# Optimization experiments

Measured on AMD Instinct MI355X. Metric: run time of the kernel, lower is better.

The kernel has to match this reference:

```python
import jax, jax.numpy as jnp
import numpy as np
import math

B, T, S, C, H = 2, 2048, 2048, 1024, 16
D = C // H  # head dim = 64


def setup_inputs() -> dict:
    key = jax.random.key(0)
    ks = jax.random.split(key, 12)
    s = 1.0 / math.sqrt(C)
    inp = {
        "query": jax.random.normal(ks[0], (B, T, C), jnp.float32),
        "key": jax.random.normal(ks[1], (B, S, C), jnp.float32),
        "value": jax.random.normal(ks[2], (B, S, C), jnp.float32),
        "Wq": jax.random.normal(ks[3], (C, C), jnp.float32) * s,
        "bq": jax.random.normal(ks[4], (C,), jnp.float32) * s,
        "Wk": jax.random.normal(ks[5], (C, C), jnp.float32) * s,
        "bk": jax.random.normal(ks[6], (C,), jnp.float32) * s,
        "Wv": jax.random.normal(ks[7], (C, C), jnp.float32) * s,
        "bv": jax.random.normal(ks[8], (C,), jnp.float32) * s,
        "Wo": jax.random.normal(ks[9], (C, C), jnp.float32) * s,
        "bo": jax.random.normal(ks[10], (C,), jnp.float32) * s,
        "query_chunk_size": 1024,
    }
    return inp


def _proj_heads(x, W, b):
    # x: [B, L, C] -> [B, H, L, D]; torch nn.Linear computes x @ W.T + b
    y = x @ W.T + b
    Bv, L, _ = y.shape
    return y.reshape(Bv, L, H, D).transpose(0, 2, 1, 3)


def reference(query, key, value, Wq, bq, Wk, bk, Wv, bv, Wo, bo, query_chunk_size):
    # query_chunk_size only controls the chunked evaluation order in the
    # original; the chunked online-softmax is mathematically identical to a
    # single stable softmax, which is what we compute here.
    q = _proj_heads(query, Wq, bq) * (1.0 / math.sqrt(D))  # [B,H,T,D]
    k = _proj_heads(key, Wk, bk)                            # [B,H,S,D]
    v = _proj_heads(value, Wv, bv)                          # [B,H,S,D]
    scores = jnp.einsum('bhqd,bhkd->bhqk', q, k)            # [B,H,T,S]
    attn = jax.nn.softmax(scores, axis=-1)
    out = jnp.einsum('bhqk,bhkd->bhqd', attn, v)            # [B,H,T,D]
    out = out.transpose(0, 2, 1, 3).reshape(query.shape[0], query.shape[1], C)
    return out @ Wo.T + bo
```

## Files before the change

kernel.cpp:

```cpp
#include <hip/hip_runtime.h>
#include <math.h>


typedef __attribute__((ext_vector_type(4))) float f32x4;
typedef __attribute__((ext_vector_type(8))) __bf16 bf16x8;
typedef __attribute__((ext_vector_type(4))) unsigned int u32x4;
typedef __attribute__((ext_vector_type(4))) unsigned short u16x4;

#define MFMA16(a, b, c) __builtin_amdgcn_mfma_f32_16x16x32_bf16(a, b, c, 0, 0, 0)

static __device__ __forceinline__ unsigned short f2bf(float f) {
    __bf16 h = (__bf16)f;
    return __builtin_bit_cast(unsigned short, h);
}

__global__ __launch_bounds__(256, 2)
void proj_qkv_kernel(const float* __restrict__ Xq, const float* __restrict__ Xk,
                     const float* __restrict__ Xv,
                     const float* __restrict__ Wq, const float* __restrict__ Wk,
                     const float* __restrict__ Wv,
                     const float* __restrict__ bq, const float* __restrict__ bk,
                     const float* __restrict__ bv,
                     unsigned short* __restrict__ qh, unsigned short* __restrict__ kh,
                     unsigned short* __restrict__ vh)
{
    const int z = blockIdx.z;
    const float* X    = (z == 0) ? Xq : (z == 1) ? Xk : Xv;
    const float* W    = (z == 0) ? Wq : (z == 1) ? Wk : Wv;
    const float* bias = (z == 0) ? bq : (z == 1) ? bk : bv;
    unsigned short* O = (z == 0) ? qh : (z == 1) ? kh : vh;
    const float scale = (z == 0) ? 0.125f : 1.0f;

    __shared__ unsigned short As[128 * 32];
    __shared__ unsigned short Bs[128 * 32];

    const int tid  = threadIdx.x;
    const int lane = tid & 63;
    const int w    = tid >> 6;
    const int l16  = lane & 15;
    const int quad = lane >> 4;
    const int wm   = (w >> 1) * 64;
    const int wn   = (w & 1) * 64;
    const int m0   = blockIdx.y * 128;
    const int n0   = blockIdx.x * 128;

    const int srow = tid >> 3;
    const int sc4  = tid & 7;

    f32x4 acc[4][4];
#pragma unroll
    for (int i = 0; i < 4; i++)
#pragma unroll
        for (int j = 0; j < 4; j++) {
            f32x4 zv = {0.0f, 0.0f, 0.0f, 0.0f};
            acc[i][j] = zv;
        }

    for (int k0 = 0; k0 < 1024; k0 += 32) {
#pragma unroll
        for (int rr = 0; rr < 4; rr++) {
            int row = rr * 32 + srow;
            f32x4 xa = *(const f32x4*)(X + (size_t)(m0 + row) * 1024 + k0 + sc4 * 4);
            f32x4 xb = *(const f32x4*)(W + (size_t)(n0 + row) * 1024 + k0 + sc4 * 4);
            u16x4 ha, hb;
#pragma unroll
            for (int e = 0; e < 4; e++) { ha[e] = f2bf(xa[e]); hb[e] = f2bf(xb[e]); }
            *(u16x4*)(As + row * 32 + sc4 * 4) = ha;
            *(u16x4*)(Bs + row * 32 + sc4 * 4) = hb;
        }
        __syncthreads();

        bf16x8 af[4], bfr[4];
#pragma unroll
        for (int mi = 0; mi < 4; mi++)
            af[mi] = *(const bf16x8*)(As + (wm + mi * 16 + l16) * 32 + quad * 8);
#pragma unroll
        for (int ni = 0; ni < 4; ni++)
            bfr[ni] = *(const bf16x8*)(Bs + (wn + ni * 16 + l16) * 32 + quad * 8);
#pragma unroll
        for (int mi = 0; mi < 4; mi++)
#pragma unroll
            for (int ni = 0; ni < 4; ni++)
                acc[mi][ni] = MFMA16(af[mi], bfr[ni], acc[mi][ni]);
        __syncthreads();
    }

#pragma unroll
    for (int ni = 0; ni < 4; ni++) {
        int gn = n0 + wn + ni * 16 + l16;
        float bval = bias[gn];
        int h = gn >> 6, d = gn & 63;
#pragma unroll
        for (int mi = 0; mi < 4; mi++) {
#pragma unroll
            for (int r = 0; r < 4; r++) {
                int gm = m0 + wm + mi * 16 + quad * 4 + r;
                int b = gm >> 11, l = gm & 2047;
                float val = (acc[mi][ni][r] + bval) * scale;
                O[(((size_t)(b * 16 + h) * 2048 + l) * 64) + d] = f2bf(val);
            }
        }
    }
}

__global__ __launch_bounds__(256, 2)
void attn_kernel(const unsigned short* __restrict__ qh,
                 const unsigned short* __restrict__ kh,
                 const unsigned short* __restrict__ vh,
                 unsigned short* __restrict__ ao)
{
    __shared__ unsigned short Vt[64 * 144];
    __shared__ unsigned short Ps[128 * 136];

    const int tid  = threadIdx.x;
    const int lane = tid & 63;
    const int w    = tid >> 6;
    const int l16  = lane & 15;
    const int quad = lane >> 4;
    const int qt   = blockIdx.x;
    const int bh   = blockIdx.y;

    const unsigned short* Qb = qh + (size_t)bh * 2048 * 64;
    const unsigned short* Kb = kh + (size_t)bh * 2048 * 64;
    const unsigned short* Vb = vh + (size_t)bh * 2048 * 64;

    bf16x8 qf[2][2];
#pragma unroll
    for (int mi = 0; mi < 2; mi++)
#pragma unroll
        for (int ks = 0; ks < 2; ks++)
            qf[mi][ks] = *(const bf16x8*)(Qb +
                (size_t)(qt * 128 + w * 32 + mi * 16 + l16) * 64 + ks * 32 + quad * 8);

    f32x4 o[2][4];
    float mrow[2][4], lrow[2][4];
#pragma unroll
    for (int mi = 0; mi < 2; mi++) {
#pragma unroll
        for (int di = 0; di < 4; di++) {
            f32x4 zv = {0.0f, 0.0f, 0.0f, 0.0f};
            o[mi][di] = zv;
        }
#pragma unroll
        for (int r = 0; r < 4; r++) { mrow[mi][r] = -__builtin_inff(); lrow[mi][r] = 0.0f; }
    }

    for (int s0 = 0; s0 < 2048; s0 += 128) {
        __syncthreads();

#pragma unroll
        for (int r = 0; r < 2; r++) {
            int p  = r * 256 + tid;
            int d0 = (p & 7) * 8;
            int sr = (p >> 3) * 2;
            const unsigned short* src = Vb + (size_t)(s0 + sr) * 64 + d0;
            u32x4 a  = *(const u32x4*)(src);
            u32x4 b2 = *(const u32x4*)(src + 64);
            unsigned int aw[4] = {a[0], a[1], a[2], a[3]};
            unsigned int bw[4] = {b2[0], b2[1], b2[2], b2[3]};
#pragma unroll
            for (int j = 0; j < 8; j++) {
                int i = (j + (p & 7)) & 7;
                unsigned int lo = (i & 1) ? (aw[i >> 1] >> 16) : (aw[i >> 1] & 0xffffu);
                unsigned int hi = (i & 1) ? (bw[i >> 1] >> 16) : (bw[i >> 1] & 0xffffu);
                *(unsigned int*)(Vt + (d0 + i) * 144 + sr) = lo | (hi << 16);
            }
        }
        __syncthreads();

        f32x4 sacc[2][8];
#pragma unroll
        for (int mi = 0; mi < 2; mi++)
#pragma unroll
            for (int ni = 0; ni < 8; ni++) {
                f32x4 zv = {0.0f, 0.0f, 0.0f, 0.0f};
                sacc[mi][ni] = zv;
            }
#pragma unroll
        for (int ni = 0; ni < 8; ni++) {
#pragma unroll
            for (int ks = 0; ks < 2; ks++) {
                bf16x8 kf = *(const bf16x8*)(Kb +
                    (size_t)(s0 + ni * 16 + l16) * 64 + ks * 32 + quad * 8);
                sacc[0][ni] = MFMA16(qf[0][ks], kf, sacc[0][ni]);
                sacc[1][ni] = MFMA16(qf[1][ks], kf, sacc[1][ni]);
            }
        }

#pragma unroll
        for (int mi = 0; mi < 2; mi++) {
#pragma unroll
            for (int r = 0; r < 4; r++) {
                float mx = sacc[mi][0][r];
#pragma unroll
                for (int ni = 1; ni < 8; ni++) mx = fmaxf(mx, sacc[mi][ni][r]);
#pragma unroll
                for (int off = 1; off < 16; off <<= 1)
                    mx = fmaxf(mx, __shfl_xor(mx, off, 64));
                float mnew  = fmaxf(mrow[mi][r], mx);
                float alpha = __expf(mrow[mi][r] - mnew);
                mrow[mi][r] = mnew;
                float sum = 0.0f;
                int prow = w * 32 + mi * 16 + quad * 4 + r;
#pragma unroll
                for (int ni = 0; ni < 8; ni++) {
                    float pv = __expf(sacc[mi][ni][r] - mnew);
                    sum += pv;
                    Ps[prow * 136 + ni * 16 + l16] = f2bf(pv);
                }
#pragma unroll
                for (int off = 1; off < 16; off <<= 1)
                    sum += __shfl_xor(sum, off, 64);
                lrow[mi][r] = lrow[mi][r] * alpha + sum;
#pragma unroll
                for (int di = 0; di < 4; di++) o[mi][di][r] *= alpha;
            }
        }

#pragma unroll
        for (int kk = 0; kk < 4; kk++) {
            bf16x8 pf[2];
#pragma unroll
            for (int mi = 0; mi < 2; mi++)
                pf[mi] = *(const bf16x8*)(Ps + (w * 32 + mi * 16 + l16) * 136 + kk * 32 + quad * 8);
#pragma unroll
            for (int di = 0; di < 4; di++) {
                bf16x8 vf = *(const bf16x8*)(Vt + (di * 16 + l16) * 144 + kk * 32 + quad * 8);
#pragma unroll
                for (int mi = 0; mi < 2; mi++)
                    o[mi][di] = MFMA16(pf[mi], vf, o[mi][di]);
            }
        }
    }

    const int b = bh >> 4, h = bh & 15;
#pragma unroll
    for (int mi = 0; mi < 2; mi++) {
#pragma unroll
        for (int r = 0; r < 4; r++) {
            float inv = 1.0f / lrow[mi][r];
            int qrow = qt * 128 + w * 32 + mi * 16 + quad * 4 + r;
#pragma unroll
            for (int di = 0; di < 4; di++) {
                float val = o[mi][di][r] * inv;
                ao[(size_t)(b * 2048 + qrow) * 1024 + h * 64 + di * 16 + l16] = f2bf(val);
            }
        }
    }
}

__global__ __launch_bounds__(256, 2)
void proj_out_kernel(const unsigned short* __restrict__ A,
                     const float* __restrict__ W,
                     const float* __restrict__ bias,
                     float* __restrict__ out)
{
    __shared__ unsigned short As[128 * 32];
    __shared__ unsigned short Bs[128 * 32];

    const int tid  = threadIdx.x;
    const int lane = tid & 63;
    const int w    = tid >> 6;
    const int l16  = lane & 15;
    const int quad = lane >> 4;
    const int wm   = (w >> 1) * 64;
    const int wn   = (w & 1) * 64;
    const int m0   = blockIdx.y * 128;
    const int n0   = blockIdx.x * 128;

    const int srow = tid >> 3;
    const int sc4  = tid & 7;

    f32x4 acc[4][4];
#pragma unroll
    for (int i = 0; i < 4; i++)
#pragma unroll
        for (int j = 0; j < 4; j++) {
            f32x4 zv = {0.0f, 0.0f, 0.0f, 0.0f};
            acc[i][j] = zv;
        }

    for (int k0 = 0; k0 < 1024; k0 += 32) {
#pragma unroll
        for (int r = 0; r < 2; r++) {
            int j = r * 256 + tid;
            int row = j >> 2, c = j & 3;
            u32x4 v = *(const u32x4*)(A + (size_t)(m0 + row) * 1024 + k0 + c * 8);
            *(u32x4*)(As + row * 32 + c * 8) = v;
        }
#pragma unroll
        for (int rr = 0; rr < 4; rr++) {
            int row = rr * 32 + srow;
            f32x4 xb = *(const f32x4*)(W + (size_t)(n0 + row) * 1024 + k0 + sc4 * 4);
            u16x4 hb;
#pragma unroll
            for (int e = 0; e < 4; e++) hb[e] = f2bf(xb[e]);
            *(u16x4*)(Bs + row * 32 + sc4 * 4) = hb;
        }
        __syncthreads();

        bf16x8 af[4], bfr[4];
#pragma unroll
        for (int mi = 0; mi < 4; mi++)
            af[mi] = *(const bf16x8*)(As + (wm + mi * 16 + l16) * 32 + quad * 8);
#pragma unroll
        for (int ni = 0; ni < 4; ni++)
            bfr[ni] = *(const bf16x8*)(Bs + (wn + ni * 16 + l16) * 32 + quad * 8);
#pragma unroll
        for (int mi = 0; mi < 4; mi++)
#pragma unroll
            for (int ni = 0; ni < 4; ni++)
                acc[mi][ni] = MFMA16(af[mi], bfr[ni], acc[mi][ni]);
        __syncthreads();
    }

#pragma unroll
    for (int ni = 0; ni < 4; ni++) {
        int gn = n0 + wn + ni * 16 + l16;
        float bval = bias[gn];
#pragma unroll
        for (int mi = 0; mi < 4; mi++) {
#pragma unroll
            for (int r = 0; r < 4; r++) {
                int gm = m0 + wm + mi * 16 + quad * 4 + r;
                out[(size_t)gm * 1024 + gn] = acc[mi][ni][r] + bval;
            }
        }
    }
}

extern "C" void kernel_launch(void* const* d_in, const int* in_sizes, int n_in,
                              void* d_out, int out_size, void* d_ws, size_t ws_size,
                              hipStream_t stream)
{
    const float* query = (const float*)d_in[0];
    const float* key   = (const float*)d_in[1];
    const float* value = (const float*)d_in[2];
    const float* Wq    = (const float*)d_in[3];
    const float* bq    = (const float*)d_in[4];
    const float* Wk    = (const float*)d_in[5];
    const float* bk    = (const float*)d_in[6];
    const float* Wv    = (const float*)d_in[7];
    const float* bv    = (const float*)d_in[8];
    const float* Wo    = (const float*)d_in[9];
    const float* bo    = (const float*)d_in[10];

    unsigned short* qh = (unsigned short*)d_ws;
    unsigned short* kh = qh + 4194304;
    unsigned short* vh = kh + 4194304;
    unsigned short* ao = vh + 4194304;
    float* out = (float*)d_out;

    proj_qkv_kernel<<<dim3(8, 32, 3), 256, 0, stream>>>(
        query, key, value, Wq, Wk, Wv, bq, bk, bv, qh, kh, vh);
    attn_kernel<<<dim3(16, 32), 256, 0, stream>>>(qh, kh, vh, ao);
    proj_out_kernel<<<dim3(8, 32), 256, 0, stream>>>(ao, Wo, bo, out);
}
```

Before: 344.1 us.

## Store V transposed from projection and restructure attention to per-wave 16-row tiles

```diff
diff --git a/kernel.cpp b/kernel.cpp
--- a/kernel.cpp
+++ b/kernel.cpp
@@ -5,6 +5,7 @@
 typedef __attribute__((ext_vector_type(4))) float f32x4;
 typedef __attribute__((ext_vector_type(8))) __bf16 bf16x8;
 typedef __attribute__((ext_vector_type(4))) unsigned int u32x4;
+typedef __attribute__((ext_vector_type(2))) unsigned int u32x2;
 typedef __attribute__((ext_vector_type(4))) unsigned short u16x4;
 
 #define MFMA16(a, b, c) __builtin_amdgcn_mfma_f32_16x16x32_bf16(a, b, c, 0, 0, 0)
@@ -12,6 +13,9 @@
 static __device__ __forceinline__ unsigned short f2bf(float f) {
     __bf16 h = (__bf16)f;
     return __builtin_bit_cast(unsigned short, h);
+}
+static __device__ __forceinline__ unsigned int pack2bf(float a, float b) {
+    return (unsigned int)f2bf(a) | ((unsigned int)f2bf(b) << 16);
 }
 
 __global__ __launch_bounds__(256, 2)
@@ -22,13 +26,13 @@
                      const float* __restrict__ bq, const float* __restrict__ bk,
                      const float* __restrict__ bv,
                      unsigned short* __restrict__ qh, unsigned short* __restrict__ kh,
-                     unsigned short* __restrict__ vh)
+                     unsigned short* __restrict__ vt)
 {
     const int z = blockIdx.z;
     const float* X    = (z == 0) ? Xq : (z == 1) ? Xk : Xv;
     const float* W    = (z == 0) ? Wq : (z == 1) ? Wk : Wv;
     const float* bias = (z == 0) ? bq : (z == 1) ? bk : bv;
-    unsigned short* O = (z == 0) ? qh : (z == 1) ? kh : vh;
+    unsigned short* O = (z == 0) ? qh : (z == 1) ? kh : vt;
     const float scale = (z == 0) ? 0.125f : 1.0f;
 
     __shared__ unsigned short As[128 * 32];
@@ -77,40 +81,66 @@
 #pragma unroll
         for (int ni = 0; ni < 4; ni++)
             bfr[ni] = *(const bf16x8*)(Bs + (wn + ni * 16 + l16) * 32 + quad * 8);
-#pragma unroll
-        for (int mi = 0; mi < 4; mi++)
-#pragma unroll
-            for (int ni = 0; ni < 4; ni++)
-                acc[mi][ni] = MFMA16(af[mi], bfr[ni], acc[mi][ni]);
+        if (z != 2) {
+#pragma unroll
+            for (int mi = 0; mi < 4; mi++)
+#pragma unroll
+                for (int ni = 0; ni < 4; ni++)
+                    acc[mi][ni] = MFMA16(af[mi], bfr[ni], acc[mi][ni]);
+        } else {
+#pragma unroll
+            for (int mi = 0; mi < 4; mi++)
+#pragma unroll
+                for (int ni = 0; ni < 4; ni++)
+                    acc[mi][ni] = MFMA16(bfr[ni], af[mi], acc[mi][ni]);
+        }
         __syncthreads();
     }
 
-#pragma unroll
-    for (int ni = 0; ni < 4; ni++) {
-        int gn = n0 + wn + ni * 16 + l16;
-        float bval = bias[gn];
-        int h = gn >> 6, d = gn & 63;
-#pragma unroll
-        for (int mi = 0; mi < 4; mi++) {
+    if (z != 2) {
+#pragma unroll
+        for (int ni = 0; ni < 4; ni++) {
+            int gn = n0 + wn + ni * 16 + l16;
+            float bval = bias[gn];
+            int h = gn >> 6, d = gn & 63;
+#pragma unroll
+            for (int mi = 0; mi < 4; mi++) {
+#pragma unroll
+                for (int r = 0; r < 4; r++) {
+                    int gm = m0 + wm + mi * 16 + quad * 4 + r;
+                    int b = gm >> 11, l = gm & 2047;
+                    float val = (acc[mi][ni][r] + bval) * scale;
+                    O[(((size_t)(b * 16 + h) * 2048 + l) * 64) + d] = f2bf(val);
+                }
+            }
+        }
+    } else {
+#pragma unroll
+        for (int ni = 0; ni < 4; ni++) {
 #pragma unroll
             for (int r = 0; r < 4; r++) {
-                int gm = m0 + wm + mi * 16 + quad * 4 + r;
-                int b = gm >> 11, l = gm & 2047;
-                float val = (acc[mi][ni][r] + bval) * scale;
-                O[(((size_t)(b * 16 + h) * 2048 + l) * 64) + d] = f2bf(val);
-            }
-        }
-    }
-}
-
-__global__ __launch_bounds__(256, 2)
+                int gn = n0 + wn + ni * 16 + quad * 4 + r;
+                float bval = bias[gn];
+                int h = gn >> 6, d = gn & 63;
+#pragma unroll
+                for (int mi = 0; mi < 4; mi++) {
+                    int gm = m0 + wm + mi * 16 + l16;
+                    int b = gm >> 11, l = gm & 2047;
+                    O[((size_t)(b * 16 + h) * 64 + d) * 2048 + l] =
+                        f2bf(acc[mi][ni][r] + bval);
+                }
+            }
+        }
+    }
+}
+
+__global__ __launch_bounds__(256, 4)
 void attn_kernel(const unsigned short* __restrict__ qh,
                  const unsigned short* __restrict__ kh,
-                 const unsigned short* __restrict__ vh,
+                 const unsigned short* __restrict__ vt,
                  unsigned short* __restrict__ ao)
 {
-    __shared__ unsigned short Vt[64 * 144];
-    __shared__ unsigned short Ps[128 * 136];
+    __shared__ unsigned short Ps[4 * 1024];
 
     const int tid  = threadIdx.x;
     const int lane = tid & 63;
@@ -122,130 +152,98 @@
 
     const unsigned short* Qb = qh + (size_t)bh * 2048 * 64;
     const unsigned short* Kb = kh + (size_t)bh * 2048 * 64;
-    const unsigned short* Vb = vh + (size_t)bh * 2048 * 64;
-
-    bf16x8 qf[2][2];
-#pragma unroll
-    for (int mi = 0; mi < 2; mi++)
-#pragma unroll
-        for (int ks = 0; ks < 2; ks++)
-            qf[mi][ks] = *(const bf16x8*)(Qb +
-                (size_t)(qt * 128 + w * 32 + mi * 16 + l16) * 64 + ks * 32 + quad * 8);
-
-    f32x4 o[2][4];
-    float mrow[2][4], lrow[2][4];
-#pragma unroll
-    for (int mi = 0; mi < 2; mi++) {
-#pragma unroll
-        for (int di = 0; di < 4; di++) {
+    const unsigned short* Vb = vt + (size_t)bh * 64 * 2048;
+
+    const int q = qt * 64 + w * 16 + l16;
+
+    bf16x8 qf[2];
+#pragma unroll
+    for (int ks = 0; ks < 2; ks++)
+        qf[ks] = *(const bf16x8*)(Qb + (size_t)q * 64 + ks * 32 + quad * 8);
+
+    f32x4 oacc[4];
+#pragma unroll
+    for (int di = 0; di < 4; di++) {
+        f32x4 zv = {0.0f, 0.0f, 0.0f, 0.0f};
+        oacc[di] = zv;
+    }
+    float m_ = -__builtin_inff(), l_ = 0.0f;
+
+    unsigned short* Pw = Ps + w * 1024;
+
+    for (int s0 = 0; s0 < 2048; s0 += 64) {
+        f32x4 sacc[4];
+#pragma unroll
+        for (int si = 0; si < 4; si++) {
             f32x4 zv = {0.0f, 0.0f, 0.0f, 0.0f};
-            o[mi][di] = zv;
-        }
-#pragma unroll
-        for (int r = 0; r < 4; r++) { mrow[mi][r] = -__builtin_inff(); lrow[mi][r] = 0.0f; }
-    }
-
-    for (int s0 = 0; s0 < 2048; s0 += 128) {
-        __syncthreads();
-
-#pragma unroll
-        for (int r = 0; r < 2; r++) {
-            int p  = r * 256 + tid;
-            int d0 = (p & 7) * 8;
-            int sr = (p >> 3) * 2;
-            const unsigned short* src = Vb + (size_t)(s0 + sr) * 64 + d0;
-            u32x4 a  = *(const u32x4*)(src);
-            u32x4 b2 = *(const u32x4*)(src + 64);
-            unsigned int aw[4] = {a[0], a[1], a[2], a[3]};
-            unsigned int bw[4] = {b2[0], b2[1], b2[2], b2[3]};
-#pragma unroll
-            for (int j = 0; j < 8; j++) {
-                int i = (j + (p & 7)) & 7;
-                unsigned int lo = (i & 1) ? (aw[i >> 1] >> 16) : (aw[i >> 1] & 0xffffu);
-                unsigned int hi = (i & 1) ? (bw[i >> 1] >> 16) : (bw[i >> 1] & 0xffffu);
-                *(unsigned int*)(Vt + (d0 + i) * 144 + sr) = lo | (hi << 16);
-            }
-        }
-        __syncthreads();
-
-        f32x4 sacc[2][8];
-#pragma unroll
-        for (int mi = 0; mi < 2; mi++)
-#pragma unroll
-            for (int ni = 0; ni < 8; ni++) {
-                f32x4 zv = {0.0f, 0.0f, 0.0f, 0.0f};
-                sacc[mi][ni] = zv;
-            }
-#pragma unroll
-        for (int ni = 0; ni < 8; ni++) {
-#pragma unroll
-            for (int ks = 0; ks < 2; ks++) {
-                bf16x8 kf = *(const bf16x8*)(Kb +
-                    (size_t)(s0 + ni * 16 + l16) * 64 + ks * 32 + quad * 8);
-                sacc[0][ni] = MFMA16(qf[0][ks], kf, sacc[0][ni]);
-                sacc[1][ni] = MFMA16(qf[1][ks], kf, sacc[1][ni]);
-            }
-        }
-
-#pragma unroll
-        for (int mi = 0; mi < 2; mi++) {
+            sacc[si] = zv;
+        }
+#pragma unroll
+        for (int si = 0; si < 4; si++) {
+            const unsigned short* kp = Kb + (size_t)(s0 + si * 16 + l16) * 64 + quad * 8;
+            bf16x8 kf0 = *(const bf16x8*)(kp);
+            bf16x8 kf1 = *(const bf16x8*)(kp + 32);
+            sacc[si] = MFMA16(kf0, qf[0], sacc[si]);
+            sacc[si] = MFMA16(kf1, qf[1], sacc[si]);
+        }
+
+        float mx = sacc[0][0];
+#pragma unroll
+        for (int si = 0; si < 4; si++)
+#pragma unroll
+            for (int r = 0; r < 4; r++) mx = fmaxf(mx, sacc[si][r]);
+        mx = fmaxf(mx, __shfl_xor(mx, 16, 64));
+        mx = fmaxf(mx, __shfl_xor(mx, 32, 64));
+        float mnew  = fmaxf(m_, mx);
+        float alpha = __expf(m_ - mnew);
+        m_ = mnew;
+        float sum = 0.0f;
+#pragma unroll
+        for (int si = 0; si < 4; si++)
 #pragma unroll
             for (int r = 0; r < 4; r++) {
-                float mx = sacc[mi][0][r];
-#pragma unroll
-                for (int ni = 1; ni < 8; ni++) mx = fmaxf(mx, sacc[mi][ni][r]);
-#pragma unroll
-                for (int off = 1; off < 16; off <<= 1)
-                    mx = fmaxf(mx, __shfl_xor(mx, off, 64));
-                float mnew  = fmaxf(mrow[mi][r], mx);
-                float alpha = __expf(mrow[mi][r] - mnew);
-                mrow[mi][r] = mnew;
-                float sum = 0.0f;
-                int prow = w * 32 + mi * 16 + quad * 4 + r;
-#pragma unroll
-                for (int ni = 0; ni < 8; ni++) {
-                    float pv = __expf(sacc[mi][ni][r] - mnew);
-                    sum += pv;
-                    Ps[prow * 136 + ni * 16 + l16] = f2bf(pv);
-                }
-#pragma unroll
-                for (int off = 1; off < 16; off <<= 1)
-                    sum += __shfl_xor(sum, off, 64);
-                lrow[mi][r] = lrow[mi][r] * alpha + sum;
-#pragma unroll
-                for (int di = 0; di < 4; di++) o[mi][di][r] *= alpha;
-            }
-        }
-
-#pragma unroll
-        for (int kk = 0; kk < 4; kk++) {
-            bf16x8 pf[2];
-#pragma unroll
-            for (int mi = 0; mi < 2; mi++)
-                pf[mi] = *(const bf16x8*)(Ps + (w * 32 + mi * 16 + l16) * 136 + kk * 32 + quad * 8);
+                float p = __expf(sacc[si][r] - mnew);
+                sacc[si][r] = p;
+                sum += p;
+            }
+        sum += __shfl_xor(sum, 16, 64);
+        sum += __shfl_xor(sum, 32, 64);
+        l_ = l_ * alpha + sum;
+#pragma unroll
+        for (int di = 0; di < 4; di++)
+#pragma unroll
+            for (int r = 0; r < 4; r++) oacc[di][r] *= alpha;
+
+#pragma unroll
+        for (int si = 0; si < 4; si++) {
+            int sc    = si >> 1;
+            int quadp = (si & 1) * 2 + (quad >> 1);
+            u32x2 dw;
+            dw[0] = pack2bf(sacc[si][0], sacc[si][1]);
+            dw[1] = pack2bf(sacc[si][2], sacc[si][3]);
+            *(u32x2*)(Pw + (sc * 64 + quadp * 16 + l16) * 8 + (quad & 1) * 4) = dw;
+        }
+
+#pragma unroll
+        for (int sc = 0; sc < 2; sc++) {
+            bf16x8 pf = *(const bf16x8*)(Pw + (sc * 64 + lane) * 8);
 #pragma unroll
             for (int di = 0; di < 4; di++) {
-                bf16x8 vf = *(const bf16x8*)(Vt + (di * 16 + l16) * 144 + kk * 32 + quad * 8);
-#pragma unroll
-                for (int mi = 0; mi < 2; mi++)
-                    o[mi][di] = MFMA16(pf[mi], vf, o[mi][di]);
+                bf16x8 vf = *(const bf16x8*)(Vb + (size_t)(di * 16 + l16) * 2048 +
+                                             s0 + sc * 32 + quad * 8);
+                oacc[di] = MFMA16(vf, pf, oacc[di]);
             }
         }
     }
 
     const int b = bh >> 4, h = bh & 15;
-#pragma unroll
-    for (int mi = 0; mi < 2; mi++) {
-#pragma unroll
-        for (int r = 0; r < 4; r++) {
-            float inv = 1.0f / lrow[mi][r];
-            int qrow = qt * 128 + w * 32 + mi * 16 + quad * 4 + r;
-#pragma unroll
-            for (int di = 0; di < 4; di++) {
-                float val = o[mi][di][r] * inv;
-                ao[(size_t)(b * 2048 + qrow) * 1024 + h * 64 + di * 16 + l16] = f2bf(val);
-            }
-        }
+    float inv = 1.0f / l_;
+#pragma unroll
+    for (int di = 0; di < 4; di++) {
+        u16x4 pk;
+#pragma unroll
+        for (int r = 0; r < 4; r++) pk[r] = f2bf(oacc[di][r] * inv);
+        *(u16x4*)(ao + (size_t)(b * 2048 + q) * 1024 + h * 64 + di * 16 + quad * 4) = pk;
     }
 }
 
@@ -347,12 +345,12 @@
 
     unsigned short* qh = (unsigned short*)d_ws;
     unsigned short* kh = qh + 4194304;
-    unsigned short* vh = kh + 4194304;
-    unsigned short* ao = vh + 4194304;
+    unsigned short* vt = kh + 4194304;
+    unsigned short* ao = vt + 4194304;
     float* out = (float*)d_out;
 
     proj_qkv_kernel<<<dim3(8, 32, 3), 256, 0, stream>>>(
-        query, key, value, Wq, Wk, Wv, bq, bk, bv, qh, kh, vh);
-    attn_kernel<<<dim3(16, 32), 256, 0, stream>>>(qh, kh, vh, ao);
+        query, key, value, Wq, Wk, Wv, bq, bk, bv, qh, kh, vt);
+    attn_kernel<<<dim3(32, 32), 256, 0, stream>>>(qh, kh, vt, ao);
     proj_out_kernel<<<dim3(8, 32), 256, 0, stream>>>(ao, Wo, bo, out);
 }
```

Result: slower. 461.2 us (+34.0%).
